# Performance work log

Measured on AMD Instinct MI355X. Metric: run time of the kernel, lower is better.

## Reference

```python
import jax, jax.numpy as jnp
import numpy as np

N = 100000   # nodes
E = 1600000  # edges (avg degree 16)
D = 128      # feature width (in_feats == all hidden_feats)
G = 1024     # number of graphs for global_add_pool
L = 3        # layers
BN_EPS = 1e-5


def setup_inputs() -> dict:
    key = jax.random.key(0)
    ks = jax.random.split(key, 6)
    x = jax.random.normal(ks[0], (N, D), dtype=jnp.float32)
    edge_index = jax.random.randint(ks[1], (2, E), 0, N, dtype=jnp.int32)
    batch = jnp.sort(jax.random.randint(ks[2], (N,), 0, G, dtype=jnp.int32))
    scale = np.float32(1.0 / np.sqrt(D))
    Ws = jax.random.normal(ks[3], (L, D, D), dtype=jnp.float32) * scale   # GCNConv weights
    bs = jnp.zeros((L, D), dtype=jnp.float32)                             # GCNConv biases
    rWs = jax.random.normal(ks[4], (L, D, D), dtype=jnp.float32) * scale  # residual Linear weights
    rbs = jnp.zeros((L, D), dtype=jnp.float32)                            # residual Linear biases
    gammas = jnp.ones((L, D), dtype=jnp.float32)                          # BN affine
    betas = jnp.zeros((L, D), dtype=jnp.float32)
    return {"x": x, "edge_index": edge_index, "batch": batch,
            "Ws": Ws, "bs": bs, "rWs": rWs, "rbs": rbs,
            "gammas": gammas, "betas": betas}


def reference(x, edge_index, batch, Ws, bs, rWs, rbs, gammas, betas):
    src, dst = edge_index[0], edge_index[1]
    # normalize='False' is a truthy string in the original -> PyG GCN norm with self-loops
    loops = jnp.arange(N, dtype=src.dtype)
    src_sl = jnp.concatenate([src, loops])  # [E+N]
    dst_sl = jnp.concatenate([dst, loops])
    deg = jax.ops.segment_sum(jnp.ones(E + N, x.dtype), dst_sl, num_segments=N)
    dinv = jax.lax.rsqrt(deg)  # deg >= 1 thanks to self-loops
    norm = (dinv[src_sl] * dinv[dst_sl])[:, None]  # [E+N, 1]

    for i in range(L):
        h = x @ Ws[i]                                   # [N, D]
        msg = h[src_sl] * norm                          # gather + scale  [E+N, D]
        agg = jax.ops.segment_sum(msg, dst_sl, num_segments=N) + bs[i]
        res = jax.nn.relu(x @ rWs[i] + rbs[i])          # residual linear + ReLU
        h = agg + res
        # BatchNorm1d in training mode: batch stats (biased variance)
        mean = h.mean(axis=0)
        var = h.var(axis=0)
        x = gammas[i] * (h - mean) * jax.lax.rsqrt(var + BN_EPS) + betas[i]

    # global_add_pool over graph ids
    return jax.ops.segment_sum(x, batch, num_segments=G)  # [G, D]
```

## Files before the change

### kernel.cpp

```cpp
#include <hip/hip_runtime.h>

#define D 128
#define NLAYERS 3
#define BN_EPS 1e-5f

typedef short bf16x8 __attribute__((ext_vector_type(8)));
typedef float f32x4 __attribute__((ext_vector_type(4)));

__device__ __forceinline__ unsigned short f2bf(float f) {
    unsigned int u = __float_as_uint(f);
    u += 0x7FFFu + ((u >> 16) & 1u);
    return (unsigned short)(u >> 16);
}
__device__ __forceinline__ float bf2f(unsigned short b) {
    return __uint_as_float(((unsigned int)b) << 16);
}
__device__ __forceinline__ float bf_lo(unsigned int u) {
    return __uint_as_float(u << 16);
}
__device__ __forceinline__ float bf_hi(unsigned int u) {
    return __uint_as_float(u & 0xFFFF0000u);
}


__global__ void k_zero(int* __restrict__ cnt, int* __restrict__ gcnt,
                       int* __restrict__ stats, int N, int G, int S) {
    int i = blockIdx.x * blockDim.x + threadIdx.x;
    if (i < N) cnt[i] = 0;
    else if (i < N + G) gcnt[i - N] = 0;
    else if (i < N + G + S) stats[i - N - G] = 0;
}

__global__ void k_hist_xb(const int* __restrict__ dst, const int* __restrict__ batch,
                          const float* __restrict__ x,
                          int* __restrict__ cnt, int* __restrict__ gcnt,
                          unsigned short* __restrict__ fb, int E, int N, int n8) {
    int i = blockIdx.x * blockDim.x + threadIdx.x;
    if (i < E) {
        atomicAdd(&cnt[dst[i]], 1);
    } else if (i < E + N) {
        atomicAdd(&gcnt[batch[i - E]], 1);
    } else {
        int j = i - E - N;
        if (j < n8) {
            const float4 a = ((const float4*)x)[j * 2];
            const float4 b = ((const float4*)x)[j * 2 + 1];
            uint4 p;
            p.x = (unsigned int)f2bf(a.x) | ((unsigned int)f2bf(a.y) << 16);
            p.y = (unsigned int)f2bf(a.z) | ((unsigned int)f2bf(a.w) << 16);
            p.z = (unsigned int)f2bf(b.x) | ((unsigned int)f2bf(b.y) << 16);
            p.w = (unsigned int)f2bf(b.z) | ((unsigned int)f2bf(b.w) << 16);
            ((uint4*)fb)[j] = p;
        }
    }
}

__global__ void k_scan_partial(const int* __restrict__ cnt, int* __restrict__ bsum,
                               float* __restrict__ dinv, unsigned short* __restrict__ hb,
                               int N) {
    __shared__ int sh[256];
    int b = blockIdx.x, t = threadIdx.x;
    int base = b * 1024 + t * 4;
    int s = 0;
#pragma unroll
    for (int i = 0; i < 4; ++i) {
        int idx = base + i;
        int cv = (idx < N) ? cnt[idx] : 0;
        if (idx < N) dinv[idx] = rsqrtf((float)(cv + 1));
        s += (cv + 3) & ~3;
    }
    if (b == 0 && t < D) hb[(size_t)N * D + t] = 0;
    sh[t] = s;
    for (int ofs = 128; ofs > 0; ofs >>= 1) {
        __syncthreads();
        if (t < ofs) sh[t] += sh[t + ofs];
    }
    __syncthreads();
    if (t == 0) bsum[b] = sh[0];
}

__global__ void k_scan_small_g(const int* __restrict__ bsum, int* __restrict__ bbase, int nb,
                               const int* __restrict__ gcnt, int* __restrict__ goff,
                               int G, int N) {
    __shared__ int sh[256];
    int t = threadIdx.x;
    if (blockIdx.x == 0) {
        int v = (t < nb) ? bsum[t] : 0;
        sh[t] = v;
        __syncthreads();
        for (int ofs = 1; ofs < 256; ofs <<= 1) {
            int vv = (t >= ofs) ? sh[t - ofs] : 0;
            __syncthreads();
            sh[t] += vv;
            __syncthreads();
        }
        bbase[t] = sh[t] - v;
    } else {
        int base = t * 4;
        int v[4]; int s = 0;
#pragma unroll
        for (int i = 0; i < 4; ++i) { v[i] = (base + i < G) ? gcnt[base + i] : 0; s += v[i]; }
        sh[t] = s;
        __syncthreads();
        for (int ofs = 1; ofs < 256; ofs <<= 1) {
            int vv = (t >= ofs) ? sh[t - ofs] : 0;
            __syncthreads();
            sh[t] += vv;
            __syncthreads();
        }
        int o = sh[t] - s;
#pragma unroll
        for (int i = 0; i < 4; ++i) {
            int idx = base + i;
            if (idx < G) { goff[idx] = o; o += v[i]; }
        }
        if (t == 255) goff[G] = N;
    }
}

__global__ void k_scan_apply(const int* __restrict__ cnt, const int* __restrict__ bbase,
                             int* __restrict__ roff, int* __restrict__ cur,
                             int* __restrict__ csr, int N) {
    __shared__ int sh[256];
    int b = blockIdx.x, t = threadIdx.x;
    int base = b * 1024 + t * 4;
    int vr[4], v[4]; int s = 0;
#pragma unroll
    for (int i = 0; i < 4; ++i) {
        int cv = (base + i < N) ? cnt[base + i] : 0;
        vr[i] = cv;
        v[i] = (cv + 3) & ~3;
        s += v[i];
    }
    sh[t] = s;
    __syncthreads();
    for (int ofs = 1; ofs < 256; ofs <<= 1) {
        int vv = (t >= ofs) ? sh[t - ofs] : 0;
        __syncthreads();
        sh[t] += vv;
        __syncthreads();
    }
    int o = bbase[b] + sh[t] - s;
#pragma unroll
    for (int i = 0; i < 4; ++i) {
        int idx = base + i;
        if (idx < N) {
            roff[idx] = o; cur[idx] = o;
            for (int p = vr[i]; p < v[i]; ++p) csr[o + p] = N;
            o += v[i];
            if (idx == N - 1) roff[N] = o;
        }
    }
}

__global__ void k_fill(const int* __restrict__ src, const int* __restrict__ dst,
                       int* __restrict__ cur, int* __restrict__ csr, int E) {
    int i = blockIdx.x * blockDim.x + threadIdx.x;
    if (i < E) {
        int p = atomicAdd(&cur[dst[i]], 1);
        csr[p] = src[i];
    }
}

__global__ void k_packfold(const float* __restrict__ W, const float* __restrict__ rW,
                           const float* __restrict__ gam, const float* __restrict__ bet,
                           const float* __restrict__ stats, const float* __restrict__ rb,
                           unsigned short* __restrict__ Wp,
                           float* __restrict__ cwA, float* __restrict__ crb,
                           int first, float invN) {
    if (blockIdx.x < 128) {
        int idx = blockIdx.x * 256 + threadIdx.x;
        int m = idx >> 14;
        int i = idx & 16383;
        int k = i >> 7, col = i & 127;
        float a = 1.f;
        if (!first) {
            float mean = stats[k] * invN;
            float var = stats[D + k] * invN - mean * mean;
            a = gam[k] * rsqrtf(var + BN_EPS);
        }
        const float* src = m ? rW : W;
        float v = a * src[i];
        int frag = ((k >> 5) << 3) + (col >> 4);
        int lane = (((k & 31) >> 3) << 4) + (col & 15);
        int j = k & 7;
        Wp[(m << 14) + frag * 512 + lane * 8 + j] = f2bf(v);
    } else {
        __shared__ float csh[128];
        int t = threadIdx.x;
        if (t < D) {
            float c = 0.f;
            if (!first) {
                float mean = stats[t] * invN;
                float var = stats[D + t] * invN - mean * mean;
                float a = gam[t] * rsqrtf(var + BN_EPS);
                c = bet[t] - mean * a;
            }
            csh[t] = c;
        }
        __syncthreads();
        if (t < D) {
            float s = 0.f;
            for (int k = 0; k < D; ++k) s += csh[k] * W[k * D + t];
            cwA[t] = s;
        } else {
            int j = t - D;
            float s = rb[j];
            for (int k = 0; k < D; ++k) s += csh[k] * rW[k * D + j];
            crb[j] = s;
        }
    }
}

__global__ __launch_bounds__(256) void k_gemm_mfma(
    const unsigned short* __restrict__ fb,
    const unsigned short* __restrict__ Wp,
    const float* __restrict__ add0, const float* __restrict__ add1,
    const float* __restrict__ dinv,
    unsigned short* __restrict__ hb, unsigned short* __restrict__ rbuf, int N) {
    __shared__ unsigned short As[128 * 128];
    __shared__ unsigned short Wb[128 * 128];
    const int t = threadIdx.x;
    const int rowbase = blockIdx.x * 128;

#pragma unroll
    for (int i = 0; i < 8; ++i) {
        int ch = t + i * 256;
        int row = ch >> 4, slot = ch & 15;
        uint4 v = make_uint4(0, 0, 0, 0);
        int gr = rowbase + row;
        if (gr < N) v = *(const uint4*)(fb + (size_t)gr * D + slot * 8);
        *(uint4*)((char*)As + row * 256 + ((slot ^ (row & 7)) << 4)) = v;
    }

    const int wave = t >> 6, l = t & 63;
    const int wrow = wave * 32;
    const int lg = l >> 4, lc = l & 15;

    const int n0 = wrow + lc;
    const int n1 = wrow + 16 + lc;
    const int g0 = rowbase + n0;
    const int g1 = rowbase + n1;
    const int f0 = lg * 4;
    const int half = lg & 1;

#pragma unroll 1
    for (int m = 0; m < 2; ++m) {
        const unsigned short* wp = Wp + (m << 14);
        __syncthreads();
#pragma unroll
        for (int i = 0; i < 8; ++i) {
            int ch = t + i * 256;
            *(uint4*)((char*)Wb + ch * 16) = *(const uint4*)((const char*)wp + ch * 16);
        }
        __syncthreads();

        f32x4 acc[2][8];
#pragma unroll
        for (int nf = 0; nf < 2; ++nf)
#pragma unroll
            for (int cf = 0; cf < 8; ++cf) acc[nf][cf] = (f32x4){0.f, 0.f, 0.f, 0.f};

#pragma unroll
        for (int ks = 0; ks < 4; ++ks) {
            const int s = ks * 4 + lg;
            bf16x8 a0 = *(const bf16x8*)((const char*)As + n0 * 256 + ((s ^ (n0 & 7)) << 4));
            bf16x8 a1 = *(const bf16x8*)((const char*)As + n1 * 256 + ((s ^ (n1 & 7)) << 4));
#pragma unroll
            for (int cf = 0; cf < 8; ++cf) {
                bf16x8 b = *(const bf16x8*)((const char*)Wb + ((ks * 8 + cf) * 64 + l) * 16);
                acc[0][cf] = __builtin_amdgcn_mfma_f32_16x16x32_bf16(b, a0, acc[0][cf], 0, 0, 0);
                acc[1][cf] = __builtin_amdgcn_mfma_f32_16x16x32_bf16(b, a1, acc[1][cf], 0, 0, 0);
            }
        }

        __syncthreads();

        if (m == 0) {
            const float dv0 = (g0 < N) ? dinv[g0] : 0.f;
            const float dv1 = (g1 < N) ? dinv[g1] : 0.f;
#pragma unroll
            for (int cf = 0; cf < 8; ++cf) {
                const int fx = cf * 16 + f0;
                const float4 va = *(const float4*)(add0 + fx);
                const int slot = cf * 2 + (lg >> 1);
                uint2 p0, p1;
                p0.x = (unsigned int)f2bf((acc[0][cf][0] + va.x) * dv0) |
                       ((unsigned int)f2bf((acc[0][cf][1] + va.y) * dv0) << 16);
                p0.y = (unsigned int)f2bf((acc[0][cf][2] + va.z) * dv0) |
                       ((unsigned int)f2bf((acc[0][cf][3] + va.w) * dv0) << 16);
                p1.x = (unsigned int)f2bf((acc[1][cf][0] + va.x) * dv1) |
                       ((unsigned int)f2bf((acc[1][cf][1] + va.y) * dv1) << 16);
                p1.y = (unsigned int)f2bf((acc[1][cf][2] + va.z) * dv1) |
                       ((unsigned int)f2bf((acc[1][cf][3] + va.w) * dv1) << 16);
                *(uint2*)((char*)Wb + n0 * 256 + ((slot ^ (n0 & 7)) << 4) + half * 8) = p0;
                *(uint2*)((char*)Wb + n1 * 256 + ((slot ^ (n1 & 7)) << 4) + half * 8) = p1;
            }
        } else {
#pragma unroll
            for (int cf = 0; cf < 8; ++cf) {
                const int fx = cf * 16 + f0;
                const float4 va = *(const float4*)(add1 + fx);
                const int slot = cf * 2 + (lg >> 1);
                uint2 p0, p1;
                p0.x = (unsigned int)f2bf(fmaxf(acc[0][cf][0] + va.x, 0.f)) |
                       ((unsigned int)f2bf(fmaxf(acc[0][cf][1] + va.y, 0.f)) << 16);
                p0.y = (unsigned int)f2bf(fmaxf(acc[0][cf][2] + va.z, 0.f)) |
                       ((unsigned int)f2bf(fmaxf(acc[0][cf][3] + va.w, 0.f)) << 16);
                p1.x = (unsigned int)f2bf(fmaxf(acc[1][cf][0] + va.x, 0.f)) |
                       ((unsigned int)f2bf(fmaxf(acc[1][cf][1] + va.y, 0.f)) << 16);
                p1.y = (unsigned int)f2bf(fmaxf(acc[1][cf][2] + va.z, 0.f)) |
                       ((unsigned int)f2bf(fmaxf(acc[1][cf][3] + va.w, 0.f)) << 16);
                *(uint2*)((char*)Wb + n0 * 256 + ((slot ^ (n0 & 7)) << 4) + half * 8) = p0;
                *(uint2*)((char*)Wb + n1 * 256 + ((slot ^ (n1 & 7)) << 4) + half * 8) = p1;
            }
        }

        __syncthreads();

        unsigned short* __restrict__ dstp = (m == 0) ? hb : rbuf;
#pragma unroll
        for (int i = 0; i < 8; ++i) {
            int ch = t + i * 256;
            int row = ch >> 4, sl = ch & 15;
            int gr = rowbase + row;
            if (gr < N) {
                uint4 v = *(const uint4*)((const char*)Wb + row * 256 + ((sl ^ (row & 7)) << 4));
                *(uint4*)(dstp + (size_t)gr * D + sl * 8) = v;
            }
        }
    }
}

__global__ __launch_bounds__(256) void k_agg(
    const unsigned short* __restrict__ hb, const unsigned short* __restrict__ resb,
    unsigned short* __restrict__ fbout,
    const int* __restrict__ roff, const int* __restrict__ csr,
    const float* __restrict__ dinv, const float* __restrict__ bias,
    float* __restrict__ stats, int N, int half) {
    const int tid = threadIdx.x;
    const int lane = tid & 63;
    const int g = lane >> 4;
    const int li = lane & 15;
    const int cs = li * 8;
    const int wid = (blockIdx.x * blockDim.x + tid) >> 6;
    const int nw = (gridDim.x * blockDim.x) >> 6;

    float bv[8];
#pragma unroll
    for (int k = 0; k < 8; ++k) bv[k] = bias[cs + k];

    float s8[8], q8[8];
#pragma unroll
    for (int k = 0; k < 8; ++k) { s8[k] = 0.f; q8[k] = 0.f; }

    for (int p = wid; p < half; p += nw) {
        const int vA = p;
        const int vB = p + half;
        const bool hasB = (vB < N);
        const int begA = roff[vA];
        const int qA = (roff[vA + 1] - begA) >> 2;
        int begB = begA, qB = 0;
        if (hasB) { begB = roff[vB]; qB = (roff[vB + 1] - begB) >> 2; }

        float accA[8], accB[8];
#pragma unroll
        for (int k = 0; k < 8; ++k) { accA[k] = 0.f; accB[k] = 0.f; }

        const int mq = (qA > qB) ? qA : qB;
        for (int i = 0; i < mq; i += 2) {
            int jA0 = i < qA ? i : (qA - 1); jA0 = jA0 < 0 ? 0 : jA0;
            int jA1 = (i + 1) < qA ? (i + 1) : (qA - 1); jA1 = jA1 < 0 ? 0 : jA1;
            int jB0 = i < qB ? i : (qB - 1); jB0 = jB0 < 0 ? 0 : jB0;
            int jB1 = (i + 1) < qB ? (i + 1) : (qB - 1); jB1 = jB1 < 0 ? 0 : jB1;
            const int4 a40 = *(const int4*)(csr + begA + jA0 * 4);
            const int4 a41 = *(const int4*)(csr + begA + jA1 * 4);
            const int4 b40 = *(const int4*)(csr + begB + jB0 * 4);
            const int4 b41 = *(const int4*)(csr + begB + jB1 * 4);
            int ua0 = (g == 0) ? a40.x : (g == 1) ? a40.y : (g == 2) ? a40.z : a40.w;
            int ua1 = (g == 0) ? a41.x : (g == 1) ? a41.y : (g == 2) ? a41.z : a41.w;
            int ub0 = (g == 0) ? b40.x : (g == 1) ? b40.y : (g == 2) ? b40.z : b40.w;
            int ub1 = (g == 0) ? b41.x : (g == 1) ? b41.y : (g == 2) ? b41.z : b41.w;
            ua0 = (i < qA) ? ua0 : N;
            ua1 = (i + 1 < qA) ? ua1 : N;
            ub0 = (i < qB) ? ub0 : N;
            ub1 = (i + 1 < qB) ? ub1 : N;
            const uint4 ga0 = *(const uint4*)(hb + (size_t)ua0 * D + cs);
            const uint4 ga1 = *(const uint4*)(hb + (size_t)ua1 * D + cs);
            const uint4 gb0 = *(const uint4*)(hb + (size_t)ub0 * D + cs);
            const uint4 gb1 = *(const uint4*)(hb + (size_t)ub1 * D + cs);
            accA[0] += bf_lo(ga0.x) + bf_lo(ga1.x); accA[1] += bf_hi(ga0.x) + bf_hi(ga1.x);
            accA[2] += bf_lo(ga0.y) + bf_lo(ga1.y); accA[3] += bf_hi(ga0.y) + bf_hi(ga1.y);
            accA[4] += bf_lo(ga0.z) + bf_lo(ga1.z); accA[5] += bf_hi(ga0.z) + bf_hi(ga1.z);
            accA[6] += bf_lo(ga0.w) + bf_lo(ga1.w); accA[7] += bf_hi(ga0.w) + bf_hi(ga1.w);
            accB[0] += bf_lo(gb0.x) + bf_lo(gb1.x); accB[1] += bf_hi(gb0.x) + bf_hi(gb1.x);
            accB[2] += bf_lo(gb0.y) + bf_lo(gb1.y); accB[3] += bf_hi(gb0.y) + bf_hi(gb1.y);
            accB[4] += bf_lo(gb0.z) + bf_lo(gb1.z); accB[5] += bf_hi(gb0.z) + bf_hi(gb1.z);
            accB[6] += bf_lo(gb0.w) + bf_lo(gb1.w); accB[7] += bf_hi(gb0.w) + bf_hi(gb1.w);
        }

#pragma unroll
        for (int k = 0; k < 8; ++k) {
            accA[k] += __shfl_xor(accA[k], 16);
            accA[k] += __shfl_xor(accA[k], 32);
            accB[k] += __shfl_xor(accB[k], 16);
            accB[k] += __shfl_xor(accB[k], 32);
        }

        {
            const float dv = dinv[vA];
            const uint4 hs = *(const uint4*)(hb + (size_t)vA * D + cs);
            const uint4 rr = *(const uint4*)(resb + (size_t)vA * D + cs);
            float ox[8];
            ox[0] = (accA[0] + bf_lo(hs.x)) * dv + bv[0] + bf_lo(rr.x);
            ox[1] = (accA[1] + bf_hi(hs.x)) * dv + bv[1] + bf_hi(rr.x);
            ox[2] = (accA[2] + bf_lo(hs.y)) * dv + bv[2] + bf_lo(rr.y);
            ox[3] = (accA[3] + bf_hi(hs.y)) * dv + bv[3] + bf_hi(rr.y);
            ox[4] = (accA[4] + bf_lo(hs.z)) * dv + bv[4] + bf_lo(rr.z);
            ox[5] = (accA[5] + bf_hi(hs.z)) * dv + bv[5] + bf_hi(rr.z);
            ox[6] = (accA[6] + bf_lo(hs.w)) * dv + bv[6] + bf_lo(rr.w);
            ox[7] = (accA[7] + bf_hi(hs.w)) * dv + bv[7] + bf_hi(rr.w);
            if (g == 0) {
                uint4 pk;
                pk.x = (unsigned int)f2bf(ox[0]) | ((unsigned int)f2bf(ox[1]) << 16);
                pk.y = (unsigned int)f2bf(ox[2]) | ((unsigned int)f2bf(ox[3]) << 16);
                pk.z = (unsigned int)f2bf(ox[4]) | ((unsigned int)f2bf(ox[5]) << 16);
                pk.w = (unsigned int)f2bf(ox[6]) | ((unsigned int)f2bf(ox[7]) << 16);
                *(uint4*)(fbout + (size_t)vA * D + cs) = pk;
#pragma unroll
                for (int k = 0; k < 8; ++k) { s8[k] += ox[k]; q8[k] += ox[k] * ox[k]; }
            }
        }
        if (hasB) {
            const float dv = dinv[vB];
            const uint4 hs = *(const uint4*)(hb + (size_t)vB * D + cs);
            const uint4 rr = *(const uint4*)(resb + (size_t)vB * D + cs);
            float ox[8];
            ox[0] = (accB[0] + bf_lo(hs.x)) * dv + bv[0] + bf_lo(rr.x);
            ox[1] = (accB[1] + bf_hi(hs.x)) * dv + bv[1] + bf_hi(rr.x);
            ox[2] = (accB[2] + bf_lo(hs.y)) * dv + bv[2] + bf_lo(rr.y);
            ox[3] = (accB[3] + bf_hi(hs.y)) * dv + bv[3] + bf_hi(rr.y);
            ox[4] = (accB[4] + bf_lo(hs.z)) * dv + bv[4] + bf_lo(rr.z);
            ox[5] = (accB[5] + bf_hi(hs.z)) * dv + bv[5] + bf_hi(rr.z);
            ox[6] = (accB[6] + bf_lo(hs.w)) * dv + bv[6] + bf_lo(rr.w);
            ox[7] = (accB[7] + bf_hi(hs.w)) * dv + bv[7] + bf_hi(rr.w);
            if (g == 0) {
                uint4 pk;
                pk.x = (unsigned int)f2bf(ox[0]) | ((unsigned int)f2bf(ox[1]) << 16);
                pk.y = (unsigned int)f2bf(ox[2]) | ((unsigned int)f2bf(ox[3]) << 16);
                pk.z = (unsigned int)f2bf(ox[4]) | ((unsigned int)f2bf(ox[5]) << 16);
                pk.w = (unsigned int)f2bf(ox[6]) | ((unsigned int)f2bf(ox[7]) << 16);
                *(uint4*)(fbout + (size_t)vB * D + cs) = pk;
#pragma unroll
                for (int k = 0; k < 8; ++k) { s8[k] += ox[k]; q8[k] += ox[k] * ox[k]; }
            }
        }
    }

    __shared__ float sred[4][16][8];
    __shared__ float qred[4][16][8];
    const int w = tid >> 6;
    if (g == 0) {
#pragma unroll
        for (int k = 0; k < 8; ++k) { sred[w][li][k] = s8[k]; qred[w][li][k] = q8[k]; }
    }
    __syncthreads();
    if (tid < D) {
        const int col = tid;
        float ts = 0.f, tq = 0.f;
#pragma unroll
        for (int ww = 0; ww < 4; ++ww) {
            ts += sred[ww][col >> 3][col & 7];
            tq += qred[ww][col >> 3][col & 7];
        }
        atomicAdd(&stats[col], ts);
        atomicAdd(&stats[D + col], tq);
    }
}

__global__ void k_pool(const unsigned short* __restrict__ fb, const int* __restrict__ goff,
                       const float* __restrict__ gam, const float* __restrict__ bet,
                       const float* __restrict__ stats, float invN,
                       float* __restrict__ out) {
    int g = blockIdx.x, t = threadIdx.x;
    float mean = stats[t] * invN;
    float var = stats[D + t] * invN - mean * mean;
    float a = gam[t] * rsqrtf(var + BN_EPS);
    float c = bet[t] - mean * a;
    int beg = goff[g], end = goff[g + 1];
    float acc = 0.f;
    for (int v = beg; v < end; ++v) acc += bf2f(fb[(size_t)v * D + t]);
    out[(size_t)g * D + t] = acc * a + (float)(end - beg) * c;
}


extern "C" void kernel_launch(void* const* d_in, const int* in_sizes, int n_in,
                              void* d_out, int out_size, void* d_ws, size_t ws_size,
                              hipStream_t stream) {
    const float* x      = (const float*)d_in[0];
    const int*   ei     = (const int*)d_in[1];
    const int*   batch  = (const int*)d_in[2];
    const float* Ws     = (const float*)d_in[3];
    const float* bs     = (const float*)d_in[4];
    const float* rWs    = (const float*)d_in[5];
    const float* rbs    = (const float*)d_in[6];
    const float* gammas = (const float*)d_in[7];
    const float* betas  = (const float*)d_in[8];
    float* out = (float*)d_out;

    const int N = in_sizes[2];
    const int E = in_sizes[1] / 2;
    const int G = out_size / D;
    const int* src = ei;
    const int* dst = ei + E;
    const int EP = E + 4 * N + 8;
    const int half = (N + 1) >> 1;
    const float invN = 1.0f / (float)N;
    const int n8 = N * (D / 8);

    char* ws = (char*)d_ws;
    size_t off = 0;
    auto alloc = [&](size_t bytes) -> char* {
        char* p = ws + off;
        off += (bytes + 255) & ~(size_t)255;
        return p;
    };
    unsigned short* hb = (unsigned short*)alloc((size_t)(N + 1) * D * 2);
    unsigned short* fb = (unsigned short*)alloc((size_t)N * D * 2);
    unsigned short* rbuf = (unsigned short*)alloc((size_t)N * D * 2);
    int*   csr  = (int*)alloc((size_t)EP * 4);
    int*   roff = (int*)alloc((size_t)(N + 1) * 4);
    int*   cur  = (int*)alloc((size_t)N * 4);
    int*   cnt  = (int*)alloc((size_t)N * 4);
    float* dinv = (float*)alloc((size_t)N * 4);
    int*   gcnt = (int*)alloc((size_t)G * 4);
    int*   goff = (int*)alloc((size_t)(G + 1) * 4);
    int*   bsum = (int*)alloc(256 * 4);
    int*   bbase= (int*)alloc(256 * 4);
    float* stats= (float*)alloc((size_t)NLAYERS * 2 * D * 4);
    unsigned short* Wp = (unsigned short*)alloc((size_t)2 * D * D * 2);
    float* cwA  = (float*)alloc(D * 4);
    float* crb  = (float*)alloc(D * 4);
    (void)ws_size;

    const int S = NLAYERS * 2 * D;
    k_zero<<<(N + G + S + 255) / 256, 256, 0, stream>>>(cnt, gcnt, (int*)stats, N, G, S);
    k_hist_xb<<<(E + N + n8 + 255) / 256, 256, 0, stream>>>(dst, batch, x, cnt, gcnt,
                                                            fb, E, N, n8);

    int nb = (N + 1023) / 1024;
    k_scan_partial<<<nb, 256, 0, stream>>>(cnt, bsum, dinv, hb, N);
    k_scan_small_g<<<2, 256, 0, stream>>>(bsum, bbase, nb, gcnt, goff, G, N);
    k_scan_apply<<<nb, 256, 0, stream>>>(cnt, bbase, roff, cur, csr, N);
    k_fill<<<(E + 255) / 256, 256, 0, stream>>>(src, dst, cur, csr, E);

    for (int l = 0; l < NLAYERS; ++l) {
        const float* W  = Ws + (size_t)l * D * D;
        const float* rW = rWs + (size_t)l * D * D;
        const float* gamP = gammas + (size_t)(l > 0 ? l - 1 : 0) * D;
        const float* betP = betas + (size_t)(l > 0 ? l - 1 : 0) * D;
        const float* stP  = stats + (size_t)(l > 0 ? l - 1 : 0) * 2 * D;

        k_packfold<<<129, 256, 0, stream>>>(W, rW, gamP, betP, stP,
                                            rbs + (size_t)l * D,
                                            Wp, cwA, crb, (l == 0) ? 1 : 0, invN);

        k_gemm_mfma<<<(N + 127) / 128, 256, 0, stream>>>(fb, Wp, cwA, crb, dinv,
                                                         hb, rbuf, N);
        k_agg<<<4096, 256, 0, stream>>>(hb, rbuf, fb, roff, csr, dinv,
                                        bs + (size_t)l * D,
                                        stats + (size_t)l * 2 * D, N, half);
    }

    k_pool<<<G, 128, 0, stream>>>(fb, goff,
                                  gammas + (size_t)(NLAYERS - 1) * D,
                                  betas + (size_t)(NLAYERS - 1) * D,
                                  stats + (size_t)(NLAYERS - 1) * 2 * D,
                                  invN, out);
}
```

Measured before the change: 746.3 us.

## Split GEMM kernel across weight matrices via 2D grid with 64-row tiles

```diff
diff --git a/kernel.cpp b/kernel.cpp
--- a/kernel.cpp
+++ b/kernel.cpp
@@ -218,13 +218,15 @@
     const float* __restrict__ add0, const float* __restrict__ add1,
     const float* __restrict__ dinv,
     unsigned short* __restrict__ hb, unsigned short* __restrict__ rbuf, int N) {
-    __shared__ unsigned short As[128 * 128];
+    __shared__ unsigned short As[64 * 128];
     __shared__ unsigned short Wb[128 * 128];
     const int t = threadIdx.x;
-    const int rowbase = blockIdx.x * 128;
-
-#pragma unroll
-    for (int i = 0; i < 8; ++i) {
+    const int m = blockIdx.y;
+    const int rowbase = blockIdx.x * 64;
+    const unsigned short* wp = Wp + (m << 14);
+
+#pragma unroll
+    for (int i = 0; i < 4; ++i) {
         int ch = t + i * 256;
         int row = ch >> 4, slot = ch & 15;
         uint4 v = make_uint4(0, 0, 0, 0);
@@ -232,102 +234,78 @@
         if (gr < N) v = *(const uint4*)(fb + (size_t)gr * D + slot * 8);
         *(uint4*)((char*)As + row * 256 + ((slot ^ (row & 7)) << 4)) = v;
     }
+#pragma unroll
+    for (int i = 0; i < 8; ++i) {
+        int ch = t + i * 256;
+        *(uint4*)((char*)Wb + ch * 16) = *(const uint4*)((const char*)wp + ch * 16);
+    }
+    __syncthreads();
 
     const int wave = t >> 6, l = t & 63;
-    const int wrow = wave * 32;
+    const int wrow = wave * 16;
     const int lg = l >> 4, lc = l & 15;
-
     const int n0 = wrow + lc;
-    const int n1 = wrow + 16 + lc;
     const int g0 = rowbase + n0;
-    const int g1 = rowbase + n1;
     const int f0 = lg * 4;
     const int half = lg & 1;
 
-#pragma unroll 1
-    for (int m = 0; m < 2; ++m) {
-        const unsigned short* wp = Wp + (m << 14);
-        __syncthreads();
-#pragma unroll
-        for (int i = 0; i < 8; ++i) {
-            int ch = t + i * 256;
-            *(uint4*)((char*)Wb + ch * 16) = *(const uint4*)((const char*)wp + ch * 16);
-        }
-        __syncthreads();
-
-        f32x4 acc[2][8];
-#pragma unroll
-        for (int nf = 0; nf < 2; ++nf)
-#pragma unroll
-            for (int cf = 0; cf < 8; ++cf) acc[nf][cf] = (f32x4){0.f, 0.f, 0.f, 0.f};
-
-#pragma unroll
-        for (int ks = 0; ks < 4; ++ks) {
-            const int s = ks * 4 + lg;
-            bf16x8 a0 = *(const bf16x8*)((const char*)As + n0 * 256 + ((s ^ (n0 & 7)) << 4));
-            bf16x8 a1 = *(const bf16x8*)((const char*)As + n1 * 256 + ((s ^ (n1 & 7)) << 4));
-#pragma unroll
-            for (int cf = 0; cf < 8; ++cf) {
-                bf16x8 b = *(const bf16x8*)((const char*)Wb + ((ks * 8 + cf) * 64 + l) * 16);
-                acc[0][cf] = __builtin_amdgcn_mfma_f32_16x16x32_bf16(b, a0, acc[0][cf], 0, 0, 0);
-                acc[1][cf] = __builtin_amdgcn_mfma_f32_16x16x32_bf16(b, a1, acc[1][cf], 0, 0, 0);
-            }
-        }
-
-        __syncthreads();
-
-        if (m == 0) {
-            const float dv0 = (g0 < N) ? dinv[g0] : 0.f;
-            const float dv1 = (g1 < N) ? dinv[g1] : 0.f;
-#pragma unroll
-            for (int cf = 0; cf < 8; ++cf) {
-                const int fx = cf * 16 + f0;
-                const float4 va = *(const float4*)(add0 + fx);
-                const int slot = cf * 2 + (lg >> 1);
-                uint2 p0, p1;
-                p0.x = (unsigned int)f2bf((acc[0][cf][0] + va.x) * dv0) |
-                       ((unsigned int)f2bf((acc[0][cf][1] + va.y) * dv0) << 16);
-                p0.y = (unsigned int)f2bf((acc[0][cf][2] + va.z) * dv0) |
-                       ((unsigned int)f2bf((acc[0][cf][3] + va.w) * dv0) << 16);
-                p1.x = (unsigned int)f2bf((acc[1][cf][0] + va.x) * dv1) |
-                       ((unsigned int)f2bf((acc[1][cf][1] + va.y) * dv1) << 16);
-                p1.y = (unsigned int)f2bf((acc[1][cf][2] + va.z) * dv1) |
-                       ((unsigned int)f2bf((acc[1][cf][3] + va.w) * dv1) << 16);
-                *(uint2*)((char*)Wb + n0 * 256 + ((slot ^ (n0 & 7)) << 4) + half * 8) = p0;
-                *(uint2*)((char*)Wb + n1 * 256 + ((slot ^ (n1 & 7)) << 4) + half * 8) = p1;
-            }
-        } else {
-#pragma unroll
-            for (int cf = 0; cf < 8; ++cf) {
-                const int fx = cf * 16 + f0;
-                const float4 va = *(const float4*)(add1 + fx);
-                const int slot = cf * 2 + (lg >> 1);
-                uint2 p0, p1;
-                p0.x = (unsigned int)f2bf(fmaxf(acc[0][cf][0] + va.x, 0.f)) |
-                       ((unsigned int)f2bf(fmaxf(acc[0][cf][1] + va.y, 0.f)) << 16);
-                p0.y = (unsigned int)f2bf(fmaxf(acc[0][cf][2] + va.z, 0.f)) |
-                       ((unsigned int)f2bf(fmaxf(acc[0][cf][3] + va.w, 0.f)) << 16);
-                p1.x = (unsigned int)f2bf(fmaxf(acc[1][cf][0] + va.x, 0.f)) |
-                       ((unsigned int)f2bf(fmaxf(acc[1][cf][1] + va.y, 0.f)) << 16);
-                p1.y = (unsigned int)f2bf(fmaxf(acc[1][cf][2] + va.z, 0.f)) |
-                       ((unsigned int)f2bf(fmaxf(acc[1][cf][3] + va.w, 0.f)) << 16);
-                *(uint2*)((char*)Wb + n0 * 256 + ((slot ^ (n0 & 7)) << 4) + half * 8) = p0;
-                *(uint2*)((char*)Wb + n1 * 256 + ((slot ^ (n1 & 7)) << 4) + half * 8) = p1;
-            }
-        }
-
-        __syncthreads();
-
-        unsigned short* __restrict__ dstp = (m == 0) ? hb : rbuf;
-#pragma unroll
-        for (int i = 0; i < 8; ++i) {
-            int ch = t + i * 256;
-            int row = ch >> 4, sl = ch & 15;
-            int gr = rowbase + row;
-            if (gr < N) {
-                uint4 v = *(const uint4*)((const char*)Wb + row * 256 + ((sl ^ (row & 7)) << 4));
-                *(uint4*)(dstp + (size_t)gr * D + sl * 8) = v;
-            }
+    f32x4 acc[8];
+#pragma unroll
+    for (int cf = 0; cf < 8; ++cf) acc[cf] = (f32x4){0.f, 0.f, 0.f, 0.f};
+
+#pragma unroll
+    for (int ks = 0; ks < 4; ++ks) {
+        const int s = ks * 4 + lg;
+        bf16x8 a0 = *(const bf16x8*)((const char*)As + n0 * 256 + ((s ^ (n0 & 7)) << 4));
+#pragma unroll
+        for (int cf = 0; cf < 8; ++cf) {
+            bf16x8 b = *(const bf16x8*)((const char*)Wb + ((ks * 8 + cf) * 64 + l) * 16);
+            acc[cf] = __builtin_amdgcn_mfma_f32_16x16x32_bf16(b, a0, acc[cf], 0, 0, 0);
+        }
+    }
+
+    __syncthreads();
+
+    if (m == 0) {
+        const float dv0 = (g0 < N) ? dinv[g0] : 0.f;
+#pragma unroll
+        for (int cf = 0; cf < 8; ++cf) {
+            const int fx = cf * 16 + f0;
+            const float4 va = *(const float4*)(add0 + fx);
+            const int slot = cf * 2 + (lg >> 1);
+            uint2 p0;
+            p0.x = (unsigned int)f2bf((acc[cf][0] + va.x) * dv0) |
+                   ((unsigned int)f2bf((acc[cf][1] + va.y) * dv0) << 16);
+            p0.y = (unsigned int)f2bf((acc[cf][2] + va.z) * dv0) |
+                   ((unsigned int)f2bf((acc[cf][3] + va.w) * dv0) << 16);
+            *(uint2*)((char*)As + n0 * 256 + ((slot ^ (n0 & 7)) << 4) + half * 8) = p0;
+        }
+    } else {
+#pragma unroll
+        for (int cf = 0; cf < 8; ++cf) {
+            const int fx = cf * 16 + f0;
+            const float4 va = *(const float4*)(add1 + fx);
+            const int slot = cf * 2 + (lg >> 1);
+            uint2 p0;
+            p0.x = (unsigned int)f2bf(fmaxf(acc[cf][0] + va.x, 0.f)) |
+                   ((unsigned int)f2bf(fmaxf(acc[cf][1] + va.y, 0.f)) << 16);
+            p0.y = (unsigned int)f2bf(fmaxf(acc[cf][2] + va.z, 0.f)) |
+                   ((unsigned int)f2bf(fmaxf(acc[cf][3] + va.w, 0.f)) << 16);
+            *(uint2*)((char*)As + n0 * 256 + ((slot ^ (n0 & 7)) << 4) + half * 8) = p0;
+        }
+    }
+
+    __syncthreads();
+
+    unsigned short* __restrict__ dstp = (m == 0) ? hb : rbuf;
+#pragma unroll
+    for (int i = 0; i < 4; ++i) {
+        int ch = t + i * 256;
+        int row = ch >> 4, sl = ch & 15;
+        int gr = rowbase + row;
+        if (gr < N) {
+            uint4 v = *(const uint4*)((const char*)As + row * 256 + ((sl ^ (row & 7)) << 4));
+            *(uint4*)(dstp + (size_t)gr * D + sl * 8) = v;
         }
     }
 }
@@ -554,6 +532,7 @@
     k_scan_apply<<<nb, 256, 0, stream>>>(cnt, bbase, roff, cur, csr, N);
     k_fill<<<(E + 255) / 256, 256, 0, stream>>>(src, dst, cur, csr, E);
 
+    dim3 ggrid((N + 63) / 64, 2);
     for (int l = 0; l < NLAYERS; ++l) {
         const float* W  = Ws + (size_t)l * D * D;
         const float* rW = rWs + (size_t)l * D * D;
@@ -565,8 +544,8 @@
                                             rbs + (size_t)l * D,
                                             Wp, cwA, crb, (l == 0) ? 1 : 0, invN);
 
-        k_gemm_mfma<<<(N + 127) / 128, 256, 0, stream>>>(fb, Wp, cwA, crb, dinv,
-                                                         hb, rbuf, N);
+        k_gemm_mfma<<<ggrid, 256, 0, stream>>>(fb, Wp, cwA, crb, dinv,
+                                               hb, rbuf, N);
         k_agg<<<4096, 256, 0, stream>>>(hb, rbuf, fb, roff, csr, dinv,
                                         bs + (size_t)l * D,
                                         stats + (size_t)l * 2 * D, N, half);
```

After: 742.8 us, median of 2. Within noise of the previous version (-0.5%).
